# Performance work log

Measured on AMD Instinct MI355X. Metric: run time of the kernel, lower is better.

The kernel has to match this reference:

```python
import jax, jax.numpy as jnp
import numpy as np

N = 50000      # nodes
M = 600000     # message edges (rows of e2)
E = 1600000    # bond-graph edges
H = 128        # hidden_channels
OE = 256       # out_emb_channels
OC = 1         # out_channels
NL = 3         # num_output_layers
ED = 8         # edge_dim


def _glorot(key, shape):
    fan_in = shape[-1]
    return jax.random.normal(key, shape, jnp.float32) / jnp.sqrt(jnp.float32(fan_in))


def setup_inputs() -> dict:
    key = jax.random.key(0)
    ks = jax.random.split(key, 24)
    inp = {}
    inp["e2"] = jax.random.normal(ks[0], (M, H), jnp.float32)
    inp["i"] = jax.random.randint(ks[1], (M,), 0, N)
    inp["afe"] = jax.random.normal(ks[2], (N, 7), jnp.float32)
    inp["b_edge_index"] = jax.random.randint(ks[3], (2, E), 0, N)
    inp["b_edge_attr"] = jax.random.uniform(ks[4], (E, ED), jnp.float32)
    # lin_v: Linear(H+7, H)
    inp["lin_v_w"] = _glorot(ks[5], (H, H + 7))
    inp["lin_v_b"] = jnp.zeros((H,), jnp.float32)
    # PDNConv (shared across both calls): lin (no bias) + edge MLP 8->8->1
    inp["conv_lin_w"] = _glorot(ks[6], (H, H))
    inp["mlp_w1"] = _glorot(ks[7], (ED, ED))
    inp["mlp_b1"] = jnp.zeros((ED,), jnp.float32)
    inp["mlp_w2"] = _glorot(ks[8], (1, ED))
    inp["mlp_b2"] = jnp.zeros((1,), jnp.float32)
    # lin_up: Linear(H, OE)
    inp["lin_up_w"] = _glorot(ks[9], (OE, H))
    inp["lin_up_b"] = jnp.zeros((OE,), jnp.float32)
    # output MLP stack: NL x Linear(OE, OE)
    inp["lins_w"] = _glorot(ks[10], (NL, OE, OE))
    inp["lins_b"] = jnp.zeros((NL, OE), jnp.float32)
    # final lin: Linear(OE, OC, bias=False)
    inp["lin_w"] = _glorot(ks[11], (OC, OE))
    return inp


def reference(e2, i, afe, b_edge_index, b_edge_attr,
              lin_v_w, lin_v_b, conv_lin_w, mlp_w1, mlp_b1, mlp_w2, mlp_b2,
              lin_up_w, lin_up_b, lins_w, lins_b, lin_w):
    # v = scatter_sum(e2, i) over nodes
    v = jax.ops.segment_sum(e2, i, num_segments=N)          # [N, H]
    v = jnp.concatenate([v, afe], axis=1) @ lin_v_w.T + lin_v_b  # [N, H]

    # PDNConv edge weights (shared by both conv calls): mlp(edge_attr) -> sigmoid scalar
    h = jnp.maximum(b_edge_attr @ mlp_w1.T + mlp_b1, 0.0)
    ew = jax.nn.sigmoid(h @ mlp_w2.T + mlp_b2)[:, 0]        # [E]
    row, col = b_edge_index[0], b_edge_index[1]
    # gcn_norm (no self loops): deg over destination, symmetric normalization
    deg = jax.ops.segment_sum(ew, col, num_segments=N)
    dinv = jnp.where(deg > 0, jax.lax.rsqrt(jnp.maximum(deg, 1e-30)), 0.0)
    norm = dinv[row] * ew * dinv[col]                        # [E]

    def conv(x):
        xw = x @ conv_lin_w.T                                # [N, H]
        return jax.ops.segment_sum(xw[row] * norm[:, None], col, num_segments=N)

    v = conv(v)
    v = conv(v)
    v = jax.nn.relu(v)

    v = v @ lin_up_w.T + lin_up_b                            # [N, OE]
    for l in range(NL):
        v = jax.nn.relu(v @ lins_w[l].T + lins_b[l])
    v = v @ lin_w.T                                          # [N, OC]
    return v
```

## Files before the change

kernel.cpp:

```cpp
#include <hip/hip_runtime.h>


#define Nn 50000
#define Mm 600000
#define Ee 1600000
#define NB 196

typedef unsigned short u16;
typedef unsigned int u32;
typedef __attribute__((ext_vector_type(8))) short bh8;
typedef __attribute__((ext_vector_type(4))) float f4;

__device__ __forceinline__ float bf2f(u16 u) {
    union { u32 i; float f; } v; v.i = ((u32)u) << 16; return v.f;
}
__device__ __forceinline__ u16 f2bf(float f) {
    union { float f; u32 u; } v; v.f = f;
    return (u16)((v.u + 0x7fffu + ((v.u >> 16) & 1u)) >> 16);
}

#define GLD16(gp, lp)                                                         \
    __builtin_amdgcn_global_load_lds(                                         \
        (const __attribute__((address_space(1))) unsigned int*)(gp),          \
        (__attribute__((address_space(3))) unsigned int*)(lp), 16, 0, 0)

__global__ __launch_bounds__(256) void k_edge(
    const float* __restrict__ attr, const int* __restrict__ eidx,
    const float* __restrict__ w1, const float* __restrict__ b1,
    const float* __restrict__ w2, const float* __restrict__ b2,
    float* __restrict__ ew, float* __restrict__ deg, int* __restrict__ cntC)
{
    __shared__ float sW1[64], sB1[8], sW2[8], sB2;
    int t = threadIdx.x;
    if (t < 64) sW1[t] = w1[t];
    if (t < 8) { sB1[t] = b1[t]; sW2[t] = w2[t]; }
    if (t == 0) sB2 = b2[0];
    __syncthreads();
    int e = blockIdx.x * 256 + t;
    if (e >= Ee) return;
    float4 q0 = *(const float4*)(attr + (size_t)e * 8);
    float4 q1 = *(const float4*)(attr + (size_t)e * 8 + 4);
    float a[8] = { q0.x, q0.y, q0.z, q0.w, q1.x, q1.y, q1.z, q1.w };
    float z = sB2;
#pragma unroll
    for (int j = 0; j < 8; ++j) {
        float h = sB1[j];
#pragma unroll
        for (int k = 0; k < 8; ++k) h += a[k] * sW1[j * 8 + k];
        z += fmaxf(h, 0.f) * sW2[j];
    }
    float s = 1.f / (1.f + __expf(-z));
    ew[e] = s;
    int c = eidx[Ee + e];
    atomicAdd(&deg[c], s);
    atomicAdd(&cntC[c], 1);
}

__global__ __launch_bounds__(256) void k_cntm(const int* __restrict__ ii,
                                              int* __restrict__ cnt)
{
    int m = blockIdx.x * 256 + threadIdx.x;
    if (m < Mm) atomicAdd(&cnt[ii[m]], 1);
}

__global__ __launch_bounds__(256) void k_scanA(
    const int* __restrict__ cnt, int* __restrict__ loc, int* __restrict__ part)
{
    __shared__ int buf[256];
    int t = threadIdx.x, i = blockIdx.x * 256 + t;
    int v = (i < Nn) ? cnt[i] : 0;
    buf[t] = v;
    __syncthreads();
#pragma unroll
    for (int d = 1; d < 256; d <<= 1) {
        int x = (t >= d) ? buf[t - d] : 0;
        __syncthreads();
        buf[t] += x;
        __syncthreads();
    }
    if (i < Nn) loc[i] = buf[t] - v;
    if (t == 255) part[blockIdx.x] = buf[255];
}

__global__ __launch_bounds__(256) void k_scanB(int* __restrict__ pA,
                                               int* __restrict__ pB)
{
    int* p = blockIdx.x ? pB : pA;
    __shared__ int buf[256];
    int t = threadIdx.x;
    int v = (t < NB) ? p[t] : 0;
    buf[t] = v;
    __syncthreads();
#pragma unroll
    for (int d = 1; d < 256; d <<= 1) {
        int x = (t >= d) ? buf[t - d] : 0;
        __syncthreads();
        buf[t] += x;
        __syncthreads();
    }
    if (t < NB) p[t] = buf[t] - v;
}

__global__ __launch_bounds__(256) void k_scanC(
    const int* __restrict__ cnt, const int* __restrict__ part,
    int* __restrict__ off, int* __restrict__ cur,
    const float* __restrict__ deg, float* __restrict__ dinv)
{
    int t = threadIdx.x, i = blockIdx.x * 256 + t;
    if (i >= Nn) return;
    int v = off[i] + part[blockIdx.x];
    off[i] = v;
    cur[i] = v;
    if (i == Nn - 1) off[Nn] = v + cnt[i];
    if (dinv) {
        float d = deg[i];
        dinv[i] = (d > 0.f) ? rsqrtf(fmaxf(d, 1e-30f)) : 0.f;
    }
}

__global__ __launch_bounds__(256) void k_scatter_col(
    const int* __restrict__ eidx, const float* __restrict__ ew,
    const float* __restrict__ dinv, int* __restrict__ cur,
    int2* __restrict__ edgep)
{
    int e = blockIdx.x * 256 + threadIdx.x;
    if (e >= Ee) return;
    int r = eidx[e], c = eidx[Ee + e];
    float nm = dinv[r] * ew[e] * dinv[c];
    int idx = atomicAdd(&cur[c], 1);
    edgep[idx] = make_int2(r, __float_as_int(nm));
}

__global__ __launch_bounds__(256) void k_scatter_m(
    const int* __restrict__ ii, int* __restrict__ cur, int* __restrict__ midx)
{
    int m = blockIdx.x * 256 + threadIdx.x;
    if (m >= Mm) return;
    midx[atomicAdd(&cur[ii[m]], 1)] = m;
}

__global__ __launch_bounds__(256) void k_segsum(
    const int* __restrict__ offM, const int* __restrict__ midx,
    const float* __restrict__ e2, const float* __restrict__ afe,
    u16* __restrict__ XH, u16* __restrict__ XL)
{
    int wv = threadIdx.x >> 6, lane = threadIdx.x & 63;
    int n = blockIdx.x * 4 + wv;
    if (n >= Nn) return;
    int j0 = offM[n], j1 = offM[n + 1];
    float a0 = 0.f, a1 = 0.f;
    int j = j0;
    if (j < j1) {
        int m = midx[j];
        float2 p = *(const float2*)(e2 + (size_t)m * 128 + lane * 2);
        for (++j; j < j1; ++j) {
            int m2 = midx[j];
            float2 p2 = *(const float2*)(e2 + (size_t)m2 * 128 + lane * 2);
            a0 += p.x; a1 += p.y;
            p = p2;
        }
        a0 += p.x; a1 += p.y;
    }
    u16 h0 = f2bf(a0), h1 = f2bf(a1);
    u16 l0 = f2bf(a0 - bf2f(h0)), l1 = f2bf(a1 - bf2f(h1));
    *(u32*)&XH[(size_t)n * 160 + lane * 2] = (u32)h0 | ((u32)h1 << 16);
    *(u32*)&XL[(size_t)n * 160 + lane * 2] = (u32)l0 | ((u32)l1 << 16);
    if (lane < 32) {
        int ch = 128 + lane;
        float v = (ch < 135) ? afe[(size_t)n * 7 + (ch - 128)] : 0.f;
        u16 h = f2bf(v);
        XH[(size_t)n * 160 + ch] = h;
        XL[(size_t)n * 160 + ch] = f2bf(v - bf2f(h));
    }
}

__global__ __launch_bounds__(256) void k_splitw(
    const float* __restrict__ src, u16* __restrict__ h, u16* __restrict__ l,
    int rows, int sc, int dc)
{
    int idx = blockIdx.x * 256 + threadIdx.x;
    if (idx >= rows * dc) return;
    int r = idx / dc, c = idx % dc;
    float x = (c < sc) ? src[(size_t)r * sc + c] : 0.f;
    u16 hh = f2bf(x);
    h[idx] = hh;
    l[idx] = f2bf(x - bf2f(hh));
}

__global__ __launch_bounds__(256) void k_gemm(
    const u16* __restrict__ Ah, const u16* __restrict__ Al,
    const u16* __restrict__ Bh, const u16* __restrict__ Bl,
    const float* __restrict__ bias, u16* __restrict__ Yh, u16* __restrict__ Yl,
    int M, int K, int NO, int flags)
{
    __shared__ __align__(16) u16 sT[4][128 * 32];
    const int t = threadIdx.x;
    const int m0 = blockIdx.x * 128, n0 = blockIdx.y * 128;
    const int lane = t & 63, wv = t >> 6;
    const int wm = (wv >> 1) * 64, wn = (wv & 1) * 64;
    const int lr = lane & 15, lq = lane >> 4;
    const u16* gplane = (wv == 0) ? Ah : (wv == 1) ? Al : (wv == 2) ? Bh : Bl;
    u16* lplane = &sT[wv][0];
    const int rbase = (wv < 2) ? m0 : n0;
    const int rlim = (wv < 2) ? (M - 1) : 0x7fffffff;
    const int srow = lane >> 2;
    const int scol = (lane & 3) * 8;
    f4 acc[4][4] = {};

    for (int k0 = 0; k0 < K; k0 += 32) {
        __syncthreads();
#pragma unroll
        for (int i = 0; i < 8; ++i) {
            int grow = rbase + i * 16 + srow;
            if (grow > rlim) grow = rlim;
            const u16* gp = gplane + (size_t)grow * K + k0 + scol;
            GLD16(gp, lplane + i * 512);
        }
        __syncthreads();
        bh8 fah[4], fal[4], fbh[4], fbl[4];
#pragma unroll
        for (int i = 0; i < 4; ++i) {
            fah[i] = *(const bh8*)&sT[0][(wm + i * 16 + lr) * 32 + lq * 8];
            fal[i] = *(const bh8*)&sT[1][(wm + i * 16 + lr) * 32 + lq * 8];
            fbh[i] = *(const bh8*)&sT[2][(wn + i * 16 + lr) * 32 + lq * 8];
            fbl[i] = *(const bh8*)&sT[3][(wn + i * 16 + lr) * 32 + lq * 8];
        }
#pragma unroll
        for (int mi = 0; mi < 4; ++mi)
#pragma unroll
            for (int ni = 0; ni < 4; ++ni) {
                acc[mi][ni] = __builtin_amdgcn_mfma_f32_16x16x32_bf16(
                    fah[mi], fbh[ni], acc[mi][ni], 0, 0, 0);
                acc[mi][ni] = __builtin_amdgcn_mfma_f32_16x16x32_bf16(
                    fal[mi], fbh[ni], acc[mi][ni], 0, 0, 0);
                acc[mi][ni] = __builtin_amdgcn_mfma_f32_16x16x32_bf16(
                    fah[mi], fbl[ni], acc[mi][ni], 0, 0, 0);
            }
    }
#pragma unroll
    for (int ni = 0; ni < 4; ++ni) {
        int gn = n0 + wn + ni * 16 + lr;
        float bv = bias ? bias[gn] : 0.f;
#pragma unroll
        for (int mi = 0; mi < 4; ++mi) {
#pragma unroll
            for (int r = 0; r < 4; ++r) {
                int gm = m0 + wm + mi * 16 + lq * 4 + r;
                if (gm < M) {
                    float v = acc[mi][ni][r] + bv;
                    if (flags & 1) v = fmaxf(v, 0.f);
                    u16 h = f2bf(v);
                    Yh[(size_t)gm * NO + gn] = h;
                    if (!(flags & 2))
                        Yl[(size_t)gm * NO + gn] = f2bf(v - bf2f(h));
                }
            }
        }
    }
}

__global__ __launch_bounds__(256) void k_gather(
    const int* __restrict__ off, const int2* __restrict__ edgep,
    const u16* __restrict__ xw, u16* __restrict__ OH, u16* __restrict__ OL,
    int relu)
{
    int wv = threadIdx.x >> 6, lane = threadIdx.x & 63;
    int n = blockIdx.x * 4 + wv;
    if (n >= Nn) return;
    int j0 = off[n], j1 = off[n + 1];
    float a0 = 0.f, a1 = 0.f;
    int j = j0;
    if (j < j1) {
        int2 ep = edgep[j];
        u32 p = *(const u32*)(xw + (size_t)ep.x * 128 + lane * 2);
        for (++j; j < j1; ++j) {
            int2 ep2 = edgep[j];
            u32 p2 = *(const u32*)(xw + (size_t)ep2.x * 128 + lane * 2);
            float w = __int_as_float(ep.y);
            a0 += w * bf2f((u16)(p & 0xffff));
            a1 += w * bf2f((u16)(p >> 16));
            ep = ep2; p = p2;
        }
        float w = __int_as_float(ep.y);
        a0 += w * bf2f((u16)(p & 0xffff));
        a1 += w * bf2f((u16)(p >> 16));
    }
    if (relu) { a0 = fmaxf(a0, 0.f); a1 = fmaxf(a1, 0.f); }
    u16 h0 = f2bf(a0), h1 = f2bf(a1);
    u16 l0 = f2bf(a0 - bf2f(h0)), l1 = f2bf(a1 - bf2f(h1));
    *(u32*)&OH[(size_t)n * 128 + lane * 2] = (u32)h0 | ((u32)h1 << 16);
    *(u32*)&OL[(size_t)n * 128 + lane * 2] = (u32)l0 | ((u32)l1 << 16);
}

__global__ __launch_bounds__(256) void k_final(
    const u16* __restrict__ Sh, const u16* __restrict__ Sl,
    const float* __restrict__ lw, float* __restrict__ out)
{
    __shared__ float w[256];
    int t = threadIdx.x;
    w[t] = lw[t];
    __syncthreads();
    int n = blockIdx.x * 4 + (t >> 6);
    int lane = t & 63;
    if (n >= Nn) return;
    float s = 0.f;
#pragma unroll
    for (int g = 0; g < 2; ++g) {
        int c = g * 128 + lane * 2;
        u32 hh = *(const u32*)(Sh + (size_t)n * 256 + c);
        u32 ll = *(const u32*)(Sl + (size_t)n * 256 + c);
        float x0 = bf2f((u16)(hh & 0xffff)) + bf2f((u16)(ll & 0xffff));
        float x1 = bf2f((u16)(hh >> 16)) + bf2f((u16)(ll >> 16));
        s += x0 * w[c] + x1 * w[c + 1];
    }
#pragma unroll
    for (int d = 32; d >= 1; d >>= 1) s += __shfl_xor(s, d, 64);
    if (lane == 0) out[n] = s;
}

extern "C" void kernel_launch(void* const* d_in, const int* in_sizes, int n_in,
                              void* d_out, int out_size, void* d_ws, size_t ws_size,
                              hipStream_t stream)
{
    (void)in_sizes; (void)n_in; (void)out_size; (void)ws_size;
    const float* e2       = (const float*)d_in[0];
    const int*   iidx     = (const int*)d_in[1];
    const float* afe      = (const float*)d_in[2];
    const int*   bei      = (const int*)d_in[3];
    const float* battr    = (const float*)d_in[4];
    const float* lin_v_w  = (const float*)d_in[5];
    const float* lin_v_b  = (const float*)d_in[6];
    const float* conv_w   = (const float*)d_in[7];
    const float* w1       = (const float*)d_in[8];
    const float* b1       = (const float*)d_in[9];
    const float* w2       = (const float*)d_in[10];
    const float* b2       = (const float*)d_in[11];
    const float* lin_up_w = (const float*)d_in[12];
    const float* lin_up_b = (const float*)d_in[13];
    const float* lins_w   = (const float*)d_in[14];
    const float* lins_b   = (const float*)d_in[15];
    const float* lin_w    = (const float*)d_in[16];

    char* ws = (char*)d_ws;
    int2*  edgep = (int2*) (ws + 0);
    float* ew    = (float*)(ws + 12800000);
    int*   midx  = (int*)  (ws + 19200000);
    int*   cntC  = (int*)  (ws + 21600000);
    int*   cntM  = (int*)  (ws + 21800000);
    float* deg   = (float*)(ws + 22000000);
    int*   offC  = (int*)  (ws + 22200000);
    int*   curC  = (int*)  (ws + 22400256);
    int*   offM  = (int*)  (ws + 22600256);
    int*   curM  = (int*)  (ws + 22800512);
    float* dinv  = (float*)(ws + 23000512);
    u16*   Wh    = (u16*)  (ws + 23200512);
    u16*   Wl    = (u16*)  (ws + 23732992);
    int*   partC = (int*)  (ws + 24265472);
    int*   partM = (int*)  (ws + 24266368);
    u16*   XcatH = (u16*)  (ws + 24268800);
    u16*   XcatL = (u16*)  (ws + 40268800);
    u16*   v1h   = (u16*)  (ws + 56268800);
    u16*   v1l   = (u16*)  (ws + 69068800);
    u16*   xw    = (u16*)  (ws + 81868800);
    u16*   gh    = (u16*)  (ws + 94668800);
    u16*   gl    = (u16*)  (ws + 107468800);
    u16*   s0h   = (u16*)  (ws + 120268800);
    u16*   s0l   = (u16*)  (ws + 145868800);
    u16*   s1h   = (u16*)  (ws + 171468800);
    u16*   s1l   = (u16*)  (ws + 197068800);

    const int oWv = 0, oConv = 20480, oLup = 36864, oLins = 69632;

    hipMemsetAsync(ws + 21600000, 0, 3 * Nn * 4, stream);

    k_edge<<<(Ee + 255) / 256, 256, 0, stream>>>(battr, bei, w1, b1, w2, b2,
                                                 ew, deg, cntC);
    k_cntm<<<(Mm + 255) / 256, 256, 0, stream>>>(iidx, cntM);
    k_scanA<<<NB, 256, 0, stream>>>(cntC, offC, partC);
    k_scanA<<<NB, 256, 0, stream>>>(cntM, offM, partM);
    k_scanB<<<2, 256, 0, stream>>>(partC, partM);
    k_scanC<<<NB, 256, 0, stream>>>(cntC, partC, offC, curC, deg, dinv);
    k_scanC<<<NB, 256, 0, stream>>>(cntM, partM, offM, curM, nullptr, nullptr);
    k_scatter_col<<<(Ee + 255) / 256, 256, 0, stream>>>(bei, ew, dinv, curC,
                                                        edgep);
    k_scatter_m<<<(Mm + 255) / 256, 256, 0, stream>>>(iidx, curM, midx);
    k_segsum<<<(Nn + 3) / 4, 256, 0, stream>>>(offM, midx, e2, afe,
                                               XcatH, XcatL);

    k_splitw<<<(128 * 160 + 255) / 256, 256, 0, stream>>>(
        lin_v_w, Wh + oWv, Wl + oWv, 128, 135, 160);
    k_splitw<<<(128 * 128 + 255) / 256, 256, 0, stream>>>(
        conv_w, Wh + oConv, Wl + oConv, 128, 128, 128);
    k_splitw<<<(256 * 128 + 255) / 256, 256, 0, stream>>>(
        lin_up_w, Wh + oLup, Wl + oLup, 256, 128, 128);
    k_splitw<<<(768 * 256 + 255) / 256, 256, 0, stream>>>(
        lins_w, Wh + oLins, Wl + oLins, 768, 256, 256);

#define GEMM(XH, XL, WO, Bp, YH, YL, M_, K_, NO_, FL_)                        \
    k_gemm<<<dim3(((M_) + 127) / 128, (NO_) / 128), 256, 0, stream>>>(        \
        XH, XL, Wh + (WO), Wl + (WO), (const float*)(Bp), YH, YL,             \
        M_, K_, NO_, FL_)

    GEMM(XcatH, XcatL, oWv, lin_v_b, v1h, v1l, Nn, 160, 128, 0);
    GEMM(v1h, v1l, oConv, nullptr, xw, nullptr, Nn, 128, 128, 2);
    k_gather<<<(Nn + 3) / 4, 256, 0, stream>>>(offC, edgep, xw, gh, gl, 0);
    GEMM(gh, gl, oConv, nullptr, xw, nullptr, Nn, 128, 128, 2);
    k_gather<<<(Nn + 3) / 4, 256, 0, stream>>>(offC, edgep, xw, gh, gl, 1);
    GEMM(gh, gl, oLup, lin_up_b, s0h, s0l, Nn, 128, 256, 0);
    GEMM(s0h, s0l, oLins + 0 * 65536, lins_b + 0,   s1h, s1l, Nn, 256, 256, 1);
    GEMM(s1h, s1l, oLins + 1 * 65536, lins_b + 256, s0h, s0l, Nn, 256, 256, 1);
    GEMM(s0h, s0l, oLins + 2 * 65536, lins_b + 512, s1h, s1l, Nn, 256, 256, 1);
    k_final<<<(Nn + 3) / 4, 256, 0, stream>>>(s1h, s1l, lin_w, (float*)d_out);
#undef GEMM
}
```

Measured before the change: 1.280 ms.

## Fuse preprocessing kernels, compute degree via CSR, fuse final projection into GEMM

Merges the M-count into the edge kernel, combines the paired scan and scatter launches into single 2D-grid launches, and merges the four weight-split launches into one. The float atomic degree accumulation is replaced by a per-node CSR reduction kernel, with the normalization applied on the fly inside the gather. The last MLP GEMM now applies bias, ReLU and the final 256->1 projection in its epilogue via atomics into the zeroed output, so the last activation is never written. This cuts launch count and memory traffic but adds atomic output accumulation and extra dinv loads per edge in the gathers.

```diff
diff --git a/kernel.cpp b/kernel.cpp
--- a/kernel.cpp
+++ b/kernel.cpp
@@ -26,9 +26,10 @@
 
 __global__ __launch_bounds__(256) void k_edge(
     const float* __restrict__ attr, const int* __restrict__ eidx,
+    const int* __restrict__ ii,
     const float* __restrict__ w1, const float* __restrict__ b1,
     const float* __restrict__ w2, const float* __restrict__ b2,
-    float* __restrict__ ew, float* __restrict__ deg, int* __restrict__ cntC)
+    float* __restrict__ ew, int* __restrict__ cntC, int* __restrict__ cntM)
 {
     __shared__ float sW1[64], sB1[8], sW2[8], sB2;
     int t = threadIdx.x;
@@ -37,6 +38,7 @@
     if (t == 0) sB2 = b2[0];
     __syncthreads();
     int e = blockIdx.x * 256 + t;
+    if (e < Mm) atomicAdd(&cntM[ii[e]], 1);
     if (e >= Ee) return;
     float4 q0 = *(const float4*)(attr + (size_t)e * 8);
     float4 q1 = *(const float4*)(attr + (size_t)e * 8 + 4);
@@ -49,23 +51,17 @@
         for (int k = 0; k < 8; ++k) h += a[k] * sW1[j * 8 + k];
         z += fmaxf(h, 0.f) * sW2[j];
     }
-    float s = 1.f / (1.f + __expf(-z));
-    ew[e] = s;
-    int c = eidx[Ee + e];
-    atomicAdd(&deg[c], s);
-    atomicAdd(&cntC[c], 1);
-}
-
-__global__ __launch_bounds__(256) void k_cntm(const int* __restrict__ ii,
-                                              int* __restrict__ cnt)
-{
-    int m = blockIdx.x * 256 + threadIdx.x;
-    if (m < Mm) atomicAdd(&cnt[ii[m]], 1);
+    ew[e] = 1.f / (1.f + __expf(-z));
+    atomicAdd(&cntC[eidx[Ee + e]], 1);
 }
 
 __global__ __launch_bounds__(256) void k_scanA(
-    const int* __restrict__ cnt, int* __restrict__ loc, int* __restrict__ part)
-{
+    const int* __restrict__ cntC_, int* __restrict__ locC, int* __restrict__ partC_,
+    const int* __restrict__ cntM_, int* __restrict__ locM, int* __restrict__ partM_)
+{
+    const int* cnt = blockIdx.y ? cntM_ : cntC_;
+    int* loc  = blockIdx.y ? locM : locC;
+    int* part = blockIdx.y ? partM_ : partC_;
     __shared__ int buf[256];
     int t = threadIdx.x, i = blockIdx.x * 256 + t;
     int v = (i < Nn) ? cnt[i] : 0;
@@ -102,41 +98,52 @@
 }
 
 __global__ __launch_bounds__(256) void k_scanC(
-    const int* __restrict__ cnt, const int* __restrict__ part,
-    int* __restrict__ off, int* __restrict__ cur,
-    const float* __restrict__ deg, float* __restrict__ dinv)
-{
+    const int* __restrict__ cntC_, const int* __restrict__ partC_,
+    int* __restrict__ offC_, int* __restrict__ curC_,
+    const int* __restrict__ cntM_, const int* __restrict__ partM_,
+    int* __restrict__ offM_, int* __restrict__ curM_)
+{
+    const int* cnt  = blockIdx.y ? cntM_ : cntC_;
+    const int* part = blockIdx.y ? partM_ : partC_;
+    int* off = blockIdx.y ? offM_ : offC_;
+    int* cur = blockIdx.y ? curM_ : curC_;
     int t = threadIdx.x, i = blockIdx.x * 256 + t;
     if (i >= Nn) return;
     int v = off[i] + part[blockIdx.x];
     off[i] = v;
     cur[i] = v;
     if (i == Nn - 1) off[Nn] = v + cnt[i];
-    if (dinv) {
-        float d = deg[i];
-        dinv[i] = (d > 0.f) ? rsqrtf(fmaxf(d, 1e-30f)) : 0.f;
-    }
-}
-
-__global__ __launch_bounds__(256) void k_scatter_col(
+}
+
+__global__ __launch_bounds__(256) void k_scatter(
     const int* __restrict__ eidx, const float* __restrict__ ew,
-    const float* __restrict__ dinv, int* __restrict__ cur,
-    int2* __restrict__ edgep)
+    const int* __restrict__ ii, int* __restrict__ curC,
+    int* __restrict__ curM, int2* __restrict__ edgep, int* __restrict__ midx)
 {
     int e = blockIdx.x * 256 + threadIdx.x;
+    if (e < Mm) midx[atomicAdd(&curM[ii[e]], 1)] = e;
     if (e >= Ee) return;
-    int r = eidx[e], c = eidx[Ee + e];
-    float nm = dinv[r] * ew[e] * dinv[c];
-    int idx = atomicAdd(&cur[c], 1);
-    edgep[idx] = make_int2(r, __float_as_int(nm));
-}
-
-__global__ __launch_bounds__(256) void k_scatter_m(
-    const int* __restrict__ ii, int* __restrict__ cur, int* __restrict__ midx)
-{
-    int m = blockIdx.x * 256 + threadIdx.x;
-    if (m >= Mm) return;
-    midx[atomicAdd(&cur[ii[m]], 1)] = m;
+    int r = eidx[e];
+    float w = ew[e];
+    int idx = atomicAdd(&curC[eidx[Ee + e]], 1);
+    edgep[idx] = make_int2(r, __float_as_int(w));
+}
+
+__global__ __launch_bounds__(256) void k_deg(
+    const int* __restrict__ offC, const int2* __restrict__ edgep,
+    float* __restrict__ dinv)
+{
+    int wv = threadIdx.x >> 6, lane = threadIdx.x & 63;
+    int n = blockIdx.x * 4 + wv;
+    if (n >= Nn) return;
+    int j0 = offC[n], j1 = offC[n + 1];
+    float s = 0.f;
+    for (int j = j0 + lane; j < j1; j += 64)
+        s += __int_as_float(edgep[j].y);
+#pragma unroll
+    for (int d = 32; d >= 1; d >>= 1) s += __shfl_xor(s, d, 64);
+    if (lane == 0)
+        dinv[n] = (s > 0.f) ? rsqrtf(fmaxf(s, 1e-30f)) : 0.f;
 }
 
 __global__ __launch_bounds__(256) void k_segsum(
@@ -175,13 +182,23 @@
 }
 
 __global__ __launch_bounds__(256) void k_splitw(
-    const float* __restrict__ src, u16* __restrict__ h, u16* __restrict__ l,
-    int rows, int sc, int dc)
+    const float* __restrict__ lin_v_w, const float* __restrict__ conv_w,
+    const float* __restrict__ lin_up_w, const float* __restrict__ lins_w,
+    u16* __restrict__ h, u16* __restrict__ l)
 {
     int idx = blockIdx.x * 256 + threadIdx.x;
-    if (idx >= rows * dc) return;
-    int r = idx / dc, c = idx % dc;
-    float x = (c < sc) ? src[(size_t)r * sc + c] : 0.f;
+    if (idx >= 266240) return;
+    float x;
+    if (idx < 20480) {
+        int r = idx / 160, c = idx % 160;
+        x = (c < 135) ? lin_v_w[(size_t)r * 135 + c] : 0.f;
+    } else if (idx < 36864) {
+        x = conv_w[idx - 20480];
+    } else if (idx < 69632) {
+        x = lin_up_w[idx - 36864];
+    } else {
+        x = lins_w[idx - 69632];
+    }
     u16 hh = f2bf(x);
     h[idx] = hh;
     l[idx] = f2bf(x - bf2f(hh));
@@ -191,6 +208,7 @@
     const u16* __restrict__ Ah, const u16* __restrict__ Al,
     const u16* __restrict__ Bh, const u16* __restrict__ Bl,
     const float* __restrict__ bias, u16* __restrict__ Yh, u16* __restrict__ Yl,
+    const float* __restrict__ lw, float* __restrict__ dout,
     int M, int K, int NO, int flags)
 {
     __shared__ __align__(16) u16 sT[4][128 * 32];
@@ -237,6 +255,34 @@
                     fah[mi], fbl[ni], acc[mi][ni], 0, 0, 0);
             }
     }
+
+    if (flags & 4) {
+        float bb[4], wl4[4];
+#pragma unroll
+        for (int ni = 0; ni < 4; ++ni) {
+            int gn = n0 + wn + ni * 16 + lr;
+            bb[ni] = bias[gn];
+            wl4[ni] = lw[gn];
+        }
+#pragma unroll
+        for (int mi = 0; mi < 4; ++mi) {
+#pragma unroll
+            for (int r = 0; r < 4; ++r) {
+                int gm = m0 + wm + mi * 16 + lq * 4 + r;
+                float sdot = 0.f;
+#pragma unroll
+                for (int ni = 0; ni < 4; ++ni)
+                    sdot += fmaxf(acc[mi][ni][r] + bb[ni], 0.f) * wl4[ni];
+                sdot += __shfl_xor(sdot, 1, 64);
+                sdot += __shfl_xor(sdot, 2, 64);
+                sdot += __shfl_xor(sdot, 4, 64);
+                sdot += __shfl_xor(sdot, 8, 64);
+                if (lr == 0 && gm < M) atomicAdd(dout + gm, sdot);
+            }
+        }
+        return;
+    }
+
 #pragma unroll
     for (int ni = 0; ni < 4; ++ni) {
         int gn = n0 + wn + ni * 16 + lr;
@@ -261,27 +307,30 @@
 
 __global__ __launch_bounds__(256) void k_gather(
     const int* __restrict__ off, const int2* __restrict__ edgep,
-    const u16* __restrict__ xw, u16* __restrict__ OH, u16* __restrict__ OL,
-    int relu)
+    const float* __restrict__ dinv, const u16* __restrict__ xw,
+    u16* __restrict__ OH, u16* __restrict__ OL, int relu)
 {
     int wv = threadIdx.x >> 6, lane = threadIdx.x & 63;
     int n = blockIdx.x * 4 + wv;
     if (n >= Nn) return;
     int j0 = off[n], j1 = off[n + 1];
+    float dn = dinv[n];
     float a0 = 0.f, a1 = 0.f;
     int j = j0;
     if (j < j1) {
         int2 ep = edgep[j];
         u32 p = *(const u32*)(xw + (size_t)ep.x * 128 + lane * 2);
+        float dr = dinv[ep.x];
         for (++j; j < j1; ++j) {
             int2 ep2 = edgep[j];
             u32 p2 = *(const u32*)(xw + (size_t)ep2.x * 128 + lane * 2);
-            float w = __int_as_float(ep.y);
+            float dr2 = dinv[ep2.x];
+            float w = dr * __int_as_float(ep.y) * dn;
             a0 += w * bf2f((u16)(p & 0xffff));
             a1 += w * bf2f((u16)(p >> 16));
-            ep = ep2; p = p2;
-        }
-        float w = __int_as_float(ep.y);
+            ep = ep2; p = p2; dr = dr2;
+        }
+        float w = dr * __int_as_float(ep.y) * dn;
         a0 += w * bf2f((u16)(p & 0xffff));
         a1 += w * bf2f((u16)(p >> 16));
     }
@@ -290,32 +339,6 @@
     u16 l0 = f2bf(a0 - bf2f(h0)), l1 = f2bf(a1 - bf2f(h1));
     *(u32*)&OH[(size_t)n * 128 + lane * 2] = (u32)h0 | ((u32)h1 << 16);
     *(u32*)&OL[(size_t)n * 128 + lane * 2] = (u32)l0 | ((u32)l1 << 16);
-}
-
-__global__ __launch_bounds__(256) void k_final(
-    const u16* __restrict__ Sh, const u16* __restrict__ Sl,
-    const float* __restrict__ lw, float* __restrict__ out)
-{
-    __shared__ float w[256];
-    int t = threadIdx.x;
-    w[t] = lw[t];
-    __syncthreads();
-    int n = blockIdx.x * 4 + (t >> 6);
-    int lane = t & 63;
-    if (n >= Nn) return;
-    float s = 0.f;
-#pragma unroll
-    for (int g = 0; g < 2; ++g) {
-        int c = g * 128 + lane * 2;
-        u32 hh = *(const u32*)(Sh + (size_t)n * 256 + c);
-        u32 ll = *(const u32*)(Sl + (size_t)n * 256 + c);
-        float x0 = bf2f((u16)(hh & 0xffff)) + bf2f((u16)(ll & 0xffff));
-        float x1 = bf2f((u16)(hh >> 16)) + bf2f((u16)(ll >> 16));
-        s += x0 * w[c] + x1 * w[c + 1];
-    }
-#pragma unroll
-    for (int d = 32; d >= 1; d >>= 1) s += __shfl_xor(s, d, 64);
-    if (lane == 0) out[n] = s;
 }
 
 extern "C" void kernel_launch(void* const* d_in, const int* in_sizes, int n_in,
@@ -347,7 +370,6 @@
     int*   midx  = (int*)  (ws + 19200000);
     int*   cntC  = (int*)  (ws + 21600000);
     int*   cntM  = (int*)  (ws + 21800000);
-    float* deg   = (float*)(ws + 22000000);
     int*   offC  = (int*)  (ws + 22200000);
     int*   curC  = (int*)  (ws + 22400256);
     int*   offM  = (int*)  (ws + 22600256);
@@ -371,45 +393,47 @@
 
     const int oWv = 0, oConv = 20480, oLup = 36864, oLins = 69632;
 
-    hipMemsetAsync(ws + 21600000, 0, 3 * Nn * 4, stream);
-
-    k_edge<<<(Ee + 255) / 256, 256, 0, stream>>>(battr, bei, w1, b1, w2, b2,
-                                                 ew, deg, cntC);
-    k_cntm<<<(Mm + 255) / 256, 256, 0, stream>>>(iidx, cntM);
-    k_scanA<<<NB, 256, 0, stream>>>(cntC, offC, partC);
-    k_scanA<<<NB, 256, 0, stream>>>(cntM, offM, partM);
+    hipMemsetAsync(ws + 21600000, 0, 400000, stream);
+    hipMemsetAsync(d_out, 0, (size_t)Nn * 4, stream);
+
+    k_edge<<<(Ee + 255) / 256, 256, 0, stream>>>(battr, bei, iidx,
+                                                 w1, b1, w2, b2,
+                                                 ew, cntC, cntM);
+    k_scanA<<<dim3(NB, 2), 256, 0, stream>>>(cntC, offC, partC,
+                                             cntM, offM, partM);
     k_scanB<<<2, 256, 0, stream>>>(partC, partM);
-    k_scanC<<<NB, 256, 0, stream>>>(cntC, partC, offC, curC, deg, dinv);
-    k_scanC<<<NB, 256, 0, stream>>>(cntM, partM, offM, curM, nullptr, nullptr);
-    k_scatter_col<<<(Ee + 255) / 256, 256, 0, stream>>>(bei, ew, dinv, curC,
-                                                        edgep);
-    k_scatter_m<<<(Mm + 255) / 256, 256, 0, stream>>>(iidx, curM, midx);
+    k_scanC<<<dim3(NB, 2), 256, 0, stream>>>(cntC, partC, offC, curC,
+                                             cntM, partM, offM, curM);
+    k_scatter<<<(Ee + 255) / 256, 256, 0, stream>>>(bei, ew, iidx, curC,
+                                                    curM, edgep, midx);
+    k_deg<<<(Nn + 3) / 4, 256, 0, stream>>>(offC, edgep, dinv);
     k_segsum<<<(Nn + 3) / 4, 256, 0, stream>>>(offM, midx, e2, afe,
                                                XcatH, XcatL);
-
-    k_splitw<<<(128 * 160 + 255) / 256, 256, 0, stream>>>(
-        lin_v_w, Wh + oWv, Wl + oWv, 128, 135, 160);
-    k_splitw<<<(128 * 128 + 255) / 256, 256, 0, stream>>>(
-        conv_w, Wh + oConv, Wl + oConv, 128, 128, 128);
-    k_splitw<<<(256 * 128 + 255) / 256, 256, 0, stream>>>(
-        lin_up_w, Wh + oLup, Wl + oLup, 256, 128, 128);
-    k_splitw<<<(768 * 256 + 255) / 256, 256, 0, stream>>>(
-        lins_w, Wh + oLins, Wl + oLins, 768, 256, 256);
-
-#define GEMM(XH, XL, WO, Bp, YH, YL, M_, K_, NO_, FL_)                        \
+    k_splitw<<<(266240 + 255) / 256, 256, 0, stream>>>(
+        lin_v_w, conv_w, lin_up_w, lins_w, Wh, Wl);
+
+#define GEMM(XH, XL, WO, Bp, YH, YL, LW, DO, M_, K_, NO_, FL_)                \
     k_gemm<<<dim3(((M_) + 127) / 128, (NO_) / 128), 256, 0, stream>>>(        \
         XH, XL, Wh + (WO), Wl + (WO), (const float*)(Bp), YH, YL,             \
-        M_, K_, NO_, FL_)
-
-    GEMM(XcatH, XcatL, oWv, lin_v_b, v1h, v1l, Nn, 160, 128, 0);
-    GEMM(v1h, v1l, oConv, nullptr, xw, nullptr, Nn, 128, 128, 2);
-    k_gather<<<(Nn + 3) / 4, 256, 0, stream>>>(offC, edgep, xw, gh, gl, 0);
-    GEMM(gh, gl, oConv, nullptr, xw, nullptr, Nn, 128, 128, 2);
-    k_gather<<<(Nn + 3) / 4, 256, 0, stream>>>(offC, edgep, xw, gh, gl, 1);
-    GEMM(gh, gl, oLup, lin_up_b, s0h, s0l, Nn, 128, 256, 0);
-    GEMM(s0h, s0l, oLins + 0 * 65536, lins_b + 0,   s1h, s1l, Nn, 256, 256, 1);
-    GEMM(s1h, s1l, oLins + 1 * 65536, lins_b + 256, s0h, s0l, Nn, 256, 256, 1);
-    GEMM(s0h, s0l, oLins + 2 * 65536, lins_b + 512, s1h, s1l, Nn, 256, 256, 1);
-    k_final<<<(Nn + 3) / 4, 256, 0, stream>>>(s1h, s1l, lin_w, (float*)d_out);
+        LW, DO, M_, K_, NO_, FL_)
+
+    GEMM(XcatH, XcatL, oWv, lin_v_b, v1h, v1l, nullptr, nullptr,
+         Nn, 160, 128, 0);
+    GEMM(v1h, v1l, oConv, nullptr, xw, nullptr, nullptr, nullptr,
+         Nn, 128, 128, 2);
+    k_gather<<<(Nn + 3) / 4, 256, 0, stream>>>(offC, edgep, dinv, xw,
+                                               gh, gl, 0);
+    GEMM(gh, gl, oConv, nullptr, xw, nullptr, nullptr, nullptr,
+         Nn, 128, 128, 2);
+    k_gather<<<(Nn + 3) / 4, 256, 0, stream>>>(offC, edgep, dinv, xw,
+                                               gh, gl, 1);
+    GEMM(gh, gl, oLup, lin_up_b, s0h, s0l, nullptr, nullptr,
+         Nn, 128, 256, 0);
+    GEMM(s0h, s0l, oLins + 0 * 65536, lins_b + 0, s1h, s1l, nullptr, nullptr,
+         Nn, 256, 256, 1);
+    GEMM(s1h, s1l, oLins + 1 * 65536, lins_b + 256, s0h, s0l, nullptr, nullptr,
+         Nn, 256, 256, 1);
+    GEMM(s0h, s0l, oLins + 2 * 65536, lins_b + 512, xw, nullptr,
+         lin_w, (float*)d_out, Nn, 256, 256, 1 | 4);
 #undef GEMM
 }
```

After: 1.338 ms. +4.5%, slower.
